# Kernel tuning notes

Hardware: AMD Instinct MI355X
Metric: run time of the kernel (lower is better)

Reference implementation:

```python
import jax, jax.numpy as jnp
import numpy as np

D_MODEL = 1024
N_HEADS = 16
HEAD_DIM = D_MODEL // N_HEADS


def setup_inputs() -> dict:
    key = jax.random.key(0)
    ks = jax.random.split(key, 9)
    s = 1.0 / np.sqrt(D_MODEL)
    inp = {
        "x": jax.random.normal(ks[0], (4, 2048, D_MODEL), dtype=jnp.float32),
        "wq": jax.random.uniform(ks[1], (D_MODEL, D_MODEL), jnp.float32, -s, s),
        "bq": jax.random.uniform(ks[2], (D_MODEL,), jnp.float32, -s, s),
        "wk": jax.random.uniform(ks[3], (D_MODEL, D_MODEL), jnp.float32, -s, s),
        "bk": jax.random.uniform(ks[4], (D_MODEL,), jnp.float32, -s, s),
        "wv": jax.random.uniform(ks[5], (D_MODEL, D_MODEL), jnp.float32, -s, s),
        "bv": jax.random.uniform(ks[6], (D_MODEL,), jnp.float32, -s, s),
        "wo": jax.random.uniform(ks[7], (D_MODEL, D_MODEL), jnp.float32, -s, s),
        "bo": jax.random.uniform(ks[8], (D_MODEL,), jnp.float32, -s, s),
    }
    return inp


def reference(x, wq, bq, wk, bk, wv, bv, wo, bo):
    b, s, d = x.shape
    h, hd = N_HEADS, HEAD_DIM
    # projections (torch Linear: y = x @ W.T + b; here weights stored as [in, out])
    q = (x @ wq + bq).reshape(b, s, h, hd).transpose(0, 2, 1, 3)  # [b,h,s,hd]
    k = (x @ wk + bk).reshape(b, s, h, hd).transpose(0, 2, 1, 3)
    v = (x @ wv + bv).reshape(b, s, h, hd).transpose(0, 2, 1, 3)
    scores = jnp.einsum("bhqd,bhkd->bhqk", q, k) / jnp.sqrt(jnp.float32(hd))
    causal = jnp.tril(jnp.ones((s, s), dtype=bool))
    scores = jnp.where(causal, scores, -jnp.inf)
    weights = jax.nn.softmax(scores, axis=-1)
    attn = jnp.einsum("bhqk,bhkd->bhqd", weights, v)  # [b,h,s,hd]
    attn = attn.transpose(0, 2, 1, 3).reshape(b, s, d)
    return attn @ wo + bo
```

## Files before the change

kernel.cpp:

```cpp
#include <hip/hip_runtime.h>
#include <cstddef>

#define D_MODEL 1024
#define NH 16
#define HD 64
#define BATCH 4
#define SEQ 2048
#define MTOT (BATCH * SEQ)

typedef _Float16 half8 __attribute__((ext_vector_type(8)));
typedef _Float16 half4v __attribute__((ext_vector_type(4)));
typedef float f32x4 __attribute__((ext_vector_type(4)));

#if __has_builtin(__builtin_amdgcn_exp2f)
#define EXP2(x) __builtin_amdgcn_exp2f(x)
#else
#define EXP2(x) __expf((x)*0.69314718056f)
#endif

#define ASYNC_COPY16(g, l)                                                    \
    __builtin_amdgcn_global_load_lds(                                         \
        (__attribute__((address_space(1))) const void*)(g),                   \
        (__attribute__((address_space(3))) void*)(l), 16, 0, 0)

#define LDSFRAG(S, R, CH)                                                     \
    (*(const half8*)((const char*)(S) + ((R) << 7) +                          \
                     ((((CH) << 1)) ^ (((R) & 7) << 4))))
#define LDSWADDR(S, R, CH)                                                    \
    ((half8*)((char*)(S) + ((R) << 7) + ((((CH) << 1)) ^ (((R) & 7) << 4))))

__global__ __launch_bounds__(256) void prep(
    const float* __restrict__ x, _Float16* __restrict__ xh,
    const float* __restrict__ W0, const float* __restrict__ W1,
    const float* __restrict__ W2, const float* __restrict__ W3,
    _Float16* __restrict__ T0, _Float16* __restrict__ T1,
    _Float16* __restrict__ T2, _Float16* __restrict__ T3)
{
    __shared__ float T[64][65];
    const int bid = blockIdx.x;
    if (bid < 256) {
        const size_t base = (size_t)bid * 4096 + threadIdx.x;
#pragma unroll
        for (int it = 0; it < 16; ++it) {
            const size_t i = base + (size_t)it * 256;
            const float4* p = (const float4*)x + 2 * i;
            float4 a = p[0], b = p[1];
            half8 h;
            h[0] = (_Float16)a.x; h[1] = (_Float16)a.y; h[2] = (_Float16)a.z; h[3] = (_Float16)a.w;
            h[4] = (_Float16)b.x; h[5] = (_Float16)b.y; h[6] = (_Float16)b.z; h[7] = (_Float16)b.w;
            *((half8*)xh + i) = h;
        }
    } else {
        const int t = bid - 256;
        const int mtx = t >> 8;
        const float* W = (mtx == 0) ? W0 : (mtx == 1) ? W1 : (mtx == 2) ? W2 : W3;
        _Float16*   Wt = (mtx == 0) ? T0 : (mtx == 1) ? T1 : (mtx == 2) ? T2 : T3;
        const int tile = t & 255;
        const int k0 = (tile >> 4) * 64, n0 = (tile & 15) * 64;
        const int r = threadIdx.x >> 4, c4 = (threadIdx.x & 15) * 4;

#pragma unroll
        for (int i = 0; i < 4; ++i) {
            float4 v = *(const float4*)(W + (size_t)(k0 + r + 16 * i) * 1024 + n0 + c4);
            T[r + 16 * i][c4 + 0] = v.x; T[r + 16 * i][c4 + 1] = v.y;
            T[r + 16 * i][c4 + 2] = v.z; T[r + 16 * i][c4 + 3] = v.w;
        }
        __syncthreads();
#pragma unroll
        for (int i = 0; i < 4; ++i) {
            const int n = r + 16 * i;
            half4v h;
            h[0] = (_Float16)T[c4 + 0][n]; h[1] = (_Float16)T[c4 + 1][n];
            h[2] = (_Float16)T[c4 + 2][n]; h[3] = (_Float16)T[c4 + 3][n];
            *(half4v*)(Wt + (size_t)(n0 + n) * 1024 + k0 + c4) = h;
        }
    }
}

template <int QKV>
__global__ __launch_bounds__(256) void gemm_mfma(
    const _Float16* __restrict__ A,
    const _Float16* __restrict__ Bt0, const _Float16* __restrict__ Bt1, const _Float16* __restrict__ Bt2,
    const float* __restrict__ bi0, const float* __restrict__ bi1, const float* __restrict__ bi2,
    void* __restrict__ C0, void* __restrict__ C1, void* __restrict__ C2)
{
    const int L = blockIdx.x;
    const int y = L & 63;
    const int c_ = L >> 6;
    const int z  = QKV ? (c_ >> 3) : 0;
    const int xb = QKV ? (c_ & 7) : c_;

    const _Float16* Bt = (z == 0) ? Bt0 : (z == 1) ? Bt1 : Bt2;
    const float*   bia = (z == 0) ? bi0 : (z == 1) ? bi1 : bi2;
    void*            C = (z == 0) ? C0  : (z == 1) ? C1  : C2;

    __shared__ _Float16 As[128][64];
    __shared__ _Float16 Bs[128][64];

    const int tid  = threadIdx.x;
    const int w    = tid >> 6;
    const int lane = tid & 63;
    const int l15  = lane & 15;
    const int lg   = lane >> 4;
    const int m0 = y * 128;
    const int n0 = xb * 128;
    const int wm = (w >> 1) * 64, wn = (w & 1) * 64;

    const int rsub = lane >> 3;
    const int cswz = ((lane & 7) ^ rsub) * 8;

    const _Float16* gA = A  + (size_t)(m0 + 32 * w + rsub) * 1024 + cswz;
    const _Float16* gB = Bt + (size_t)(n0 + 32 * w + rsub) * 1024 + cswz;
    char* lA = (char*)As + (size_t)(w * 4) * 1024;
    char* lB = (char*)Bs + (size_t)(w * 4) * 1024;

    f32x4 acc[4][4];
#pragma unroll
    for (int i = 0; i < 4; ++i)
#pragma unroll
        for (int j = 0; j < 4; ++j) { acc[i][j][0] = 0.f; acc[i][j][1] = 0.f; acc[i][j][2] = 0.f; acc[i][j][3] = 0.f; }

    for (int kt = 0; kt < 16; ++kt) {
        const int k0 = kt * 64;
        __syncthreads();
#pragma unroll
        for (int i = 0; i < 4; ++i) {
            ASYNC_COPY16(gA + (size_t)(8 * i) * 1024 + k0, lA + i * 1024);
            ASYNC_COPY16(gB + (size_t)(8 * i) * 1024 + k0, lB + i * 1024);
        }
        __syncthreads();

#pragma unroll
        for (int c = 0; c < 2; ++c) {
            half8 af[4], bf[4];
#pragma unroll
            for (int i = 0; i < 4; ++i) af[i] = LDSFRAG(As, wm + 16 * i + l15, 32 * c + 8 * lg);
#pragma unroll
            for (int j = 0; j < 4; ++j) bf[j] = LDSFRAG(Bs, wn + 16 * j + l15, 32 * c + 8 * lg);
#pragma unroll
            for (int i = 0; i < 4; ++i)
#pragma unroll
                for (int j = 0; j < 4; ++j)
                    acc[i][j] = __builtin_amdgcn_mfma_f32_16x16x32_f16(af[i], bf[j], acc[i][j], 0, 0, 0);
        }
    }

    float bvv[4];
#pragma unroll
    for (int j = 0; j < 4; ++j) bvv[j] = bia[n0 + wn + 16 * j + l15];

#pragma unroll
    for (int i = 0; i < 4; ++i)
#pragma unroll
        for (int j = 0; j < 4; ++j)
#pragma unroll
            for (int r = 0; r < 4; ++r) {
                const int m = m0 + wm + 16 * i + 4 * lg + r;
                const int n = n0 + wn + 16 * j + l15;
                float val = acc[i][j][r] + bvv[j];
                if (QKV) {
                    if (z == 0) val *= 0.18033688f;
                    const int bb = m >> 11, ss = m & 2047, hh = n >> 6, hd = n & 63;
                    if (z < 2)
                        ((_Float16*)C)[((size_t)(bb * NH + hh) * SEQ + ss) * HD + hd] = (_Float16)val;
                    else
                        ((_Float16*)C)[((size_t)(bb * NH + hh) * HD + hd) * SEQ + ss] = (_Float16)val;
                } else {
                    ((float*)C)[(size_t)m * 1024 + n] = val;
                }
            }
}

__global__ __launch_bounds__(256, 3) void attn_fwd_mfma(
    const _Float16* __restrict__ Q, const _Float16* __restrict__ K,
    const _Float16* __restrict__ Vt, _Float16* __restrict__ O)
{
    __shared__ _Float16 Ks[2][64][64];
    __shared__ _Float16 Vs[2][64][64];
    __shared__ _Float16 Ps[8][16][72];

    const int tid  = threadIdx.x;
    const int w    = tid >> 6;
    const int lane = tid & 63;
    const int l15  = lane & 15;
    const int lg   = lane >> 4;

    const int bid = blockIdx.x;
    const int bh  = bid & 63;
    const int qt  = 15 - (bid >> 6);
    const int b  = bh >> 4, h = bh & 15;

    const _Float16* Qb  = Q  + (size_t)bh * SEQ * HD;
    const _Float16* Kb  = K  + (size_t)bh * SEQ * HD;
    const _Float16* Vtb = Vt + (size_t)bh * HD * SEQ;

    const int srow = tid >> 3;
    const int scol = (tid & 7) * 8;

    const int q0 = qt * 128;
    const int ntiles = 2 * qt + 2;

    half8 qa[2][2];
#pragma unroll
    for (int u = 0; u < 2; ++u) {
        const _Float16* qp = Qb + (size_t)(q0 + 16 * (2 * w + u) + l15) * HD + 8 * lg;
        qa[u][0] = *(const half8*)(qp);
        qa[u][1] = *(const half8*)(qp + 32);
    }

    f32x4 o_[2][4];
#pragma unroll
    for (int u = 0; u < 2; ++u)
#pragma unroll
        for (int ft = 0; ft < 4; ++ft) { o_[u][ft][0] = 0.f; o_[u][ft][1] = 0.f; o_[u][ft][2] = 0.f; o_[u][ft][3] = 0.f; }
    float lp_t[2] = {0.f, 0.f};

    half8 kreg[2], vreg[2];
#pragma unroll
    for (int j = 0; j < 2; ++j) {
        kreg[j] = *(const half8*)(Kb  + (size_t)(srow + 32 * j) * HD + scol);
        vreg[j] = *(const half8*)(Vtb + (size_t)(srow + 32 * j) * SEQ + scol);
    }

    for (int kt = 0; kt < ntiles; ++kt) {
        const int cur = kt & 1;
#pragma unroll
        for (int j = 0; j < 2; ++j) {
            const int row = srow + 32 * j;
            *LDSWADDR(&Ks[cur][0][0], row, scol) = kreg[j];
            *LDSWADDR(&Vs[cur][0][0], row, scol) = vreg[j];
        }
        __syncthreads();

        if (kt + 1 < ntiles) {
            const int k0 = (kt + 1) * 64;
#pragma unroll
            for (int j = 0; j < 2; ++j) {
                kreg[j] = *(const half8*)(Kb  + (size_t)(k0 + srow + 32 * j) * HD + scol);
                vreg[j] = *(const half8*)(Vtb + (size_t)(srow + 32 * j) * SEQ + k0 + scol);
            }
        }

        f32x4 s0[4], s1[4];
#pragma unroll
        for (int f = 0; f < 4; ++f) {
            s0[f][0] = 0.f; s0[f][1] = 0.f; s0[f][2] = 0.f; s0[f][3] = 0.f;
            s1[f][0] = 0.f; s1[f][1] = 0.f; s1[f][2] = 0.f; s1[f][3] = 0.f;
        }
        __builtin_amdgcn_s_setprio(1);
#pragma unroll
        for (int c = 0; c < 2; ++c)
#pragma unroll
            for (int f = 0; f < 4; ++f) {
                half8 kb = LDSFRAG(&Ks[cur][0][0], 16 * f + l15, 32 * c + 8 * lg);
                s0[f] = __builtin_amdgcn_mfma_f32_16x16x32_f16(kb, qa[0][c], s0[f], 0, 0, 0);
                s1[f] = __builtin_amdgcn_mfma_f32_16x16x32_f16(kb, qa[1][c], s1[f], 0, 0, 0);
            }
        __builtin_amdgcn_s_setprio(0);

        const bool dg = (kt >= 2 * qt);
#pragma unroll
        for (int u = 0; u < 2; ++u) {
            const int qg = q0 + 16 * (2 * w + u) + l15;
#pragma unroll
            for (int f = 0; f < 4; ++f) {
                half4v ph;
#pragma unroll
                for (int r = 0; r < 4; ++r) {
                    const float sv = (u == 0) ? s0[f][r] : s1[f][r];
                    float p = EXP2(sv);
                    if (dg && (kt * 64 + 16 * f + 4 * lg + r > qg)) p = 0.f;
                    lp_t[u] += p;
                    ph[r] = (_Float16)p;
                }
                *(half4v*)&Ps[2 * w + u][l15][16 * f + 4 * lg] = ph;
            }
        }

        half8 pa0[2], pa1[2];
        pa0[0] = *(const half8*)&Ps[2 * w][l15][8 * lg];
        pa0[1] = *(const half8*)&Ps[2 * w][l15][32 + 8 * lg];
        pa1[0] = *(const half8*)&Ps[2 * w + 1][l15][8 * lg];
        pa1[1] = *(const half8*)&Ps[2 * w + 1][l15][32 + 8 * lg];
        __builtin_amdgcn_s_setprio(1);
#pragma unroll
        for (int c = 0; c < 2; ++c)
#pragma unroll
            for (int ft = 0; ft < 4; ++ft) {
                half8 vb = LDSFRAG(&Vs[cur][0][0], 16 * ft + l15, 32 * c + 8 * lg);
                o_[0][ft] = __builtin_amdgcn_mfma_f32_16x16x32_f16(pa0[c], vb, o_[0][ft], 0, 0, 0);
                o_[1][ft] = __builtin_amdgcn_mfma_f32_16x16x32_f16(pa1[c], vb, o_[1][ft], 0, 0, 0);
            }
        __builtin_amdgcn_s_setprio(0);
    }

#pragma unroll
    for (int u = 0; u < 2; ++u) {
        float rs = lp_t[u];
        rs += __shfl_xor(rs, 16);
        rs += __shfl_xor(rs, 32);
#pragma unroll
        for (int r = 0; r < 4; ++r) {
            const float inv = 1.0f / __shfl(rs, 4 * lg + r, 64);
            _Float16* orow = O + (size_t)(b * SEQ + q0 + 16 * (2 * w + u) + 4 * lg + r) * D_MODEL + h * HD + l15;
#pragma unroll
            for (int ft = 0; ft < 4; ++ft) orow[16 * ft] = (_Float16)(o_[u][ft][r] * inv);
        }
    }
}

extern "C" void kernel_launch(void* const* d_in, const int* in_sizes, int n_in,
                              void* d_out, int out_size, void* d_ws, size_t ws_size,
                              hipStream_t stream)
{
    const float* x  = (const float*)d_in[0];
    const float* wq = (const float*)d_in[1];
    const float* bq = (const float*)d_in[2];
    const float* wk = (const float*)d_in[3];
    const float* bk = (const float*)d_in[4];
    const float* wv = (const float*)d_in[5];
    const float* bv = (const float*)d_in[6];
    const float* wo = (const float*)d_in[7];
    const float* bo = (const float*)d_in[8];
    float* out = (float*)d_out;

    const size_t SZ = (size_t)MTOT * D_MODEL;
    const size_t WZ = (size_t)D_MODEL * D_MODEL;

    _Float16* xh  = (_Float16*)d_ws;
    _Float16* wtq = xh + SZ;
    _Float16* wtk = wtq + WZ;
    _Float16* wtv = wtk + WZ;
    _Float16* wto = wtv + WZ;
    _Float16* Qh  = wto + WZ;
    _Float16* Kh  = Qh + SZ;
    _Float16* Vtg = Kh + SZ;
    _Float16* AOh = Vtg + SZ;

    prep<<<dim3(1280), 256, 0, stream>>>(x, xh, wq, wk, wv, wo, wtq, wtk, wtv, wto);
    gemm_mfma<1><<<dim3(1536), 256, 0, stream>>>(xh, wtq, wtk, wtv, bq, bk, bv, Qh, Kh, Vtg);
    attn_fwd_mfma<<<dim3(1024), 256, 0, stream>>>(Qh, Kh, Vtg, AOh);
    gemm_mfma<0><<<dim3(512), 256, 0, stream>>>(AOh, wto, wto, wto, bo, bo, bo, out, out, out);
}
```

Measured before the change: 255.6 us.

## Fuse fp32-to-fp16 conversion of x into QKV GEMM A-tile loading

After: 276.8 us. +8.3%, slower.

```diff
diff --git a/kernel.cpp b/kernel.cpp
--- a/kernel.cpp
+++ b/kernel.cpp
@@ -30,56 +30,40 @@
     ((half8*)((char*)(S) + ((R) << 7) + ((((CH) << 1)) ^ (((R) & 7) << 4))))
 
 __global__ __launch_bounds__(256) void prep(
-    const float* __restrict__ x, _Float16* __restrict__ xh,
     const float* __restrict__ W0, const float* __restrict__ W1,
     const float* __restrict__ W2, const float* __restrict__ W3,
     _Float16* __restrict__ T0, _Float16* __restrict__ T1,
     _Float16* __restrict__ T2, _Float16* __restrict__ T3)
 {
     __shared__ float T[64][65];
-    const int bid = blockIdx.x;
-    if (bid < 256) {
-        const size_t base = (size_t)bid * 4096 + threadIdx.x;
-#pragma unroll
-        for (int it = 0; it < 16; ++it) {
-            const size_t i = base + (size_t)it * 256;
-            const float4* p = (const float4*)x + 2 * i;
-            float4 a = p[0], b = p[1];
-            half8 h;
-            h[0] = (_Float16)a.x; h[1] = (_Float16)a.y; h[2] = (_Float16)a.z; h[3] = (_Float16)a.w;
-            h[4] = (_Float16)b.x; h[5] = (_Float16)b.y; h[6] = (_Float16)b.z; h[7] = (_Float16)b.w;
-            *((half8*)xh + i) = h;
-        }
-    } else {
-        const int t = bid - 256;
-        const int mtx = t >> 8;
-        const float* W = (mtx == 0) ? W0 : (mtx == 1) ? W1 : (mtx == 2) ? W2 : W3;
-        _Float16*   Wt = (mtx == 0) ? T0 : (mtx == 1) ? T1 : (mtx == 2) ? T2 : T3;
-        const int tile = t & 255;
-        const int k0 = (tile >> 4) * 64, n0 = (tile & 15) * 64;
-        const int r = threadIdx.x >> 4, c4 = (threadIdx.x & 15) * 4;
-
-#pragma unroll
-        for (int i = 0; i < 4; ++i) {
-            float4 v = *(const float4*)(W + (size_t)(k0 + r + 16 * i) * 1024 + n0 + c4);
-            T[r + 16 * i][c4 + 0] = v.x; T[r + 16 * i][c4 + 1] = v.y;
-            T[r + 16 * i][c4 + 2] = v.z; T[r + 16 * i][c4 + 3] = v.w;
-        }
-        __syncthreads();
-#pragma unroll
-        for (int i = 0; i < 4; ++i) {
-            const int n = r + 16 * i;
-            half4v h;
-            h[0] = (_Float16)T[c4 + 0][n]; h[1] = (_Float16)T[c4 + 1][n];
-            h[2] = (_Float16)T[c4 + 2][n]; h[3] = (_Float16)T[c4 + 3][n];
-            *(half4v*)(Wt + (size_t)(n0 + n) * 1024 + k0 + c4) = h;
-        }
+    const int t = blockIdx.x;
+    const int mtx = t >> 8;
+    const float* W = (mtx == 0) ? W0 : (mtx == 1) ? W1 : (mtx == 2) ? W2 : W3;
+    _Float16*   Wt = (mtx == 0) ? T0 : (mtx == 1) ? T1 : (mtx == 2) ? T2 : T3;
+    const int tile = t & 255;
+    const int k0 = (tile >> 4) * 64, n0 = (tile & 15) * 64;
+    const int r = threadIdx.x >> 4, c4 = (threadIdx.x & 15) * 4;
+
+#pragma unroll
+    for (int i = 0; i < 4; ++i) {
+        float4 v = *(const float4*)(W + (size_t)(k0 + r + 16 * i) * 1024 + n0 + c4);
+        T[r + 16 * i][c4 + 0] = v.x; T[r + 16 * i][c4 + 1] = v.y;
+        T[r + 16 * i][c4 + 2] = v.z; T[r + 16 * i][c4 + 3] = v.w;
+    }
+    __syncthreads();
+#pragma unroll
+    for (int i = 0; i < 4; ++i) {
+        const int n = r + 16 * i;
+        half4v h;
+        h[0] = (_Float16)T[c4 + 0][n]; h[1] = (_Float16)T[c4 + 1][n];
+        h[2] = (_Float16)T[c4 + 2][n]; h[3] = (_Float16)T[c4 + 3][n];
+        *(half4v*)(Wt + (size_t)(n0 + n) * 1024 + k0 + c4) = h;
     }
 }
 
 template <int QKV>
 __global__ __launch_bounds__(256) void gemm_mfma(
-    const _Float16* __restrict__ A,
+    const void* __restrict__ Ap,
     const _Float16* __restrict__ Bt0, const _Float16* __restrict__ Bt1, const _Float16* __restrict__ Bt2,
     const float* __restrict__ bi0, const float* __restrict__ bi1, const float* __restrict__ bi2,
     void* __restrict__ C0, void* __restrict__ C1, void* __restrict__ C2)
@@ -109,26 +93,66 @@
     const int rsub = lane >> 3;
     const int cswz = ((lane & 7) ^ rsub) * 8;
 
-    const _Float16* gA = A  + (size_t)(m0 + 32 * w + rsub) * 1024 + cswz;
+    const int srow  = tid >> 3;
+    const int scol8 = (tid & 7) * 8;
+
     const _Float16* gB = Bt + (size_t)(n0 + 32 * w + rsub) * 1024 + cswz;
+    char* lB = (char*)Bs + (size_t)(w * 4) * 1024;
+
+    const float*    gx = (const float*)Ap + (size_t)(m0 + srow) * 1024 + scol8;
+    const _Float16* gA = (const _Float16*)Ap + (size_t)(m0 + 32 * w + rsub) * 1024 + cswz;
     char* lA = (char*)As + (size_t)(w * 4) * 1024;
-    char* lB = (char*)Bs + (size_t)(w * 4) * 1024;
 
     f32x4 acc[4][4];
 #pragma unroll
     for (int i = 0; i < 4; ++i)
 #pragma unroll
         for (int j = 0; j < 4; ++j) { acc[i][j][0] = 0.f; acc[i][j][1] = 0.f; acc[i][j][2] = 0.f; acc[i][j][3] = 0.f; }
+
+    float4 axr[4][2];
+    if constexpr (QKV) {
+#pragma unroll
+        for (int j = 0; j < 4; ++j) {
+            axr[j][0] = *(const float4*)(gx + (size_t)(32 * j) * 1024);
+            axr[j][1] = *(const float4*)(gx + (size_t)(32 * j) * 1024 + 4);
+        }
+    }
 
     for (int kt = 0; kt < 16; ++kt) {
         const int k0 = kt * 64;
         __syncthreads();
-#pragma unroll
-        for (int i = 0; i < 4; ++i) {
-            ASYNC_COPY16(gA + (size_t)(8 * i) * 1024 + k0, lA + i * 1024);
+
+        if constexpr (QKV) {
+#pragma unroll
+            for (int j = 0; j < 4; ++j) {
+                half8 h;
+                h[0] = (_Float16)axr[j][0].x; h[1] = (_Float16)axr[j][0].y;
+                h[2] = (_Float16)axr[j][0].z; h[3] = (_Float16)axr[j][0].w;
+                h[4] = (_Float16)axr[j][1].x; h[5] = (_Float16)axr[j][1].y;
+                h[6] = (_Float16)axr[j][1].z; h[7] = (_Float16)axr[j][1].w;
+                *LDSWADDR(As, srow + 32 * j, scol8) = h;
+            }
+        } else {
+#pragma unroll
+            for (int i = 0; i < 4; ++i)
+                ASYNC_COPY16(gA + (size_t)(8 * i) * 1024 + k0, lA + i * 1024);
+        }
+#pragma unroll
+        for (int i = 0; i < 4; ++i)
             ASYNC_COPY16(gB + (size_t)(8 * i) * 1024 + k0, lB + i * 1024);
-        }
+
         __syncthreads();
+
+        if constexpr (QKV) {
+            if (kt < 15) {
+                const int k0n = k0 + 64;
+#pragma unroll
+                for (int j = 0; j < 4; ++j) {
+                    axr[j][0] = *(const float4*)(gx + (size_t)(32 * j) * 1024 + k0n);
+                    axr[j][1] = *(const float4*)(gx + (size_t)(32 * j) * 1024 + k0n + 4);
+                }
+            }
+        }
 
 #pragma unroll
         for (int c = 0; c < 2; ++c) {
@@ -327,8 +351,7 @@
     const size_t SZ = (size_t)MTOT * D_MODEL;
     const size_t WZ = (size_t)D_MODEL * D_MODEL;
 
-    _Float16* xh  = (_Float16*)d_ws;
-    _Float16* wtq = xh + SZ;
+    _Float16* wtq = (_Float16*)d_ws;
     _Float16* wtk = wtq + WZ;
     _Float16* wtv = wtk + WZ;
     _Float16* wto = wtv + WZ;
@@ -337,8 +360,8 @@
     _Float16* Vtg = Kh + SZ;
     _Float16* AOh = Vtg + SZ;
 
-    prep<<<dim3(1280), 256, 0, stream>>>(x, xh, wq, wk, wv, wo, wtq, wtk, wtv, wto);
-    gemm_mfma<1><<<dim3(1536), 256, 0, stream>>>(xh, wtq, wtk, wtv, bq, bk, bv, Qh, Kh, Vtg);
+    prep<<<dim3(1024), 256, 0, stream>>>(wq, wk, wv, wo, wtq, wtk, wtv, wto);
+    gemm_mfma<1><<<dim3(1536), 256, 0, stream>>>(x, wtq, wtk, wtv, bq, bk, bv, Qh, Kh, Vtg);
     attn_fwd_mfma<<<dim3(1024), 256, 0, stream>>>(Qh, Kh, Vtg, AOh);
     gemm_mfma<0><<<dim3(512), 256, 0, stream>>>(AOh, wto, wto, wto, bo, bo, bo, out, out, out);
 }
```
